# Performance work log

Measured on AMD Instinct MI355X. Metric: run time of the kernel, lower is better.

The kernel has to match this reference:

```python
import jax, jax.numpy as jnp
import numpy as np

B, T, D, H, V, L = 2, 1024, 512, 8, 50257, 4
HD = D // H  # head size
FF = 4 * D


def _ln(x, w, b):
    mu = jnp.mean(x, axis=-1, keepdims=True)
    var = jnp.mean((x - mu) ** 2, axis=-1, keepdims=True)
    return (x - mu) * jax.lax.rsqrt(var + 1e-5) * w + b


def setup_inputs() -> dict:
    key = jax.random.key(0)
    ks = jax.random.split(key, 12)
    s = 0.02
    return {
        "idx": jax.random.randint(ks[0], (B, T), 0, V),
        "tok_emb": jax.random.normal(ks[1], (V, D)) * s,
        "pos_emb": jax.random.normal(ks[2], (T, D)) * s,
        "Wq": jax.random.normal(ks[3], (L, H, D, HD)) * s,
        "Wk": jax.random.normal(ks[4], (L, H, D, HD)) * s,
        "Wv": jax.random.normal(ks[5], (L, H, D, HD)) * s,
        "Wo": jax.random.normal(ks[6], (L, D, D)) * s,
        "bo": jnp.zeros((L, D)),
        "W1": jax.random.normal(ks[7], (L, D, FF)) * s,
        "b1": jnp.zeros((L, FF)),
        "W2": jax.random.normal(ks[8], (L, FF, D)) * s,
        "b2": jnp.zeros((L, D)),
        "ln1_w": jnp.ones((L, D)), "ln1_b": jnp.zeros((L, D)),
        "ln2_w": jnp.ones((L, D)), "ln2_b": jnp.zeros((L, D)),
        "Wlm": jax.random.normal(ks[9], (D, V)) * s,
        "blm": jnp.zeros((V,)),
    }


def reference(idx, tok_emb, pos_emb, Wq, Wk, Wv, Wo, bo, W1, b1, W2, b2,
              ln1_w, ln1_b, ln2_w, ln2_b, Wlm, blm):
    b, t = idx.shape
    x = tok_emb[idx] + pos_emb[:t]  # [B,T,D]
    mask = jnp.tril(jnp.ones((t, t), dtype=bool))
    scale = D ** (-0.5)  # NOTE: original scales by full n_embd, not head_size
    for l in range(L):
        # pre-norm that also feeds the residual (x = ln1(x); x = x + sa(x))
        h = _ln(x, ln1_w[l], ln1_b[l])
        q = jnp.einsum('btd,hdk->bhtk', h, Wq[l])
        k = jnp.einsum('btd,hdk->bhtk', h, Wk[l])
        v = jnp.einsum('btd,hdk->bhtk', h, Wv[l])
        wei = jnp.einsum('bhtk,bhsk->bhts', q, k) * scale
        wei = jnp.where(mask, wei, -jnp.inf)
        wei = jax.nn.softmax(wei, axis=-1)  # dropout omitted (eval mode)
        att = jnp.einsum('bhts,bhsk->bhtk', wei, v)
        att = att.transpose(0, 2, 1, 3).reshape(b, t, D)  # concat heads
        x = h + att @ Wo[l] + bo[l]
        h2 = _ln(x, ln2_w[l], ln2_b[l])
        x = h2 + jax.nn.relu(h2 @ W1[l] + b1[l]) @ W2[l] + b2[l]
    logits = x @ Wlm + blm  # [B,T,V]
    return logits
```

## Files before the change

### kernel.cpp

```cpp
#include <hip/hip_runtime.h>
#include <hip/hip_bf16.h>

typedef __hip_bfloat16 bf16;
typedef __attribute__((ext_vector_type(8))) short s8v;
typedef __attribute__((ext_vector_type(4))) float f4v;

#define B_ 2
#define T_ 1024
#define D_ 512
#define H_ 8
#define HD_ 64
#define V_ 50257
#define VPAD_ 51200
#define L_ 4
#define FF_ 2048
#define BT_ (B_*T_)

__device__ __forceinline__ float ldw(const void* p, size_t i, int f32m) {
  return f32m ? ((const float*)p)[i] : __bfloat162float(((const bf16*)p)[i]);
}

__device__ __forceinline__ void gload_lds16(const void* g, void* l) {
  __builtin_amdgcn_global_load_lds((const __attribute__((address_space(1))) void*)g,
                                   (__attribute__((address_space(3))) void*)l, 16, 0, 0);
}

__global__ void detect_kernel(const void* __restrict__ ln1w, int* __restrict__ flag) {
  unsigned u = *(const unsigned*)ln1w;
  *flag = (u == 0x3F800000u) ? 1 : 0;
}

__global__ void embed_kernel(const int* __restrict__ idx, const void* __restrict__ tok,
                             const void* __restrict__ pos, float* __restrict__ x,
                             const int* __restrict__ flag) {
  int f32m = *flag;
  int i = blockIdx.x * 256 + threadIdx.x;
  int bt = i >> 9;
  int d  = i & (D_ - 1);
  int t  = bt & (T_ - 1);
  int tk = idx[bt];
  x[i] = ldw(tok, (size_t)tk * D_ + d, f32m) + ldw(pos, (size_t)t * D_ + d, f32m);
}

__global__ void ln_kernel(const float* __restrict__ x, const void* __restrict__ w,
                          const void* __restrict__ b, size_t eoff,
                          bf16* __restrict__ hb, float* __restrict__ hf,
                          const int* __restrict__ flag) {
  int f32m = *flag;
  int t = blockIdx.x;
  int tid = threadIdx.x;
  const float* row = x + (size_t)t * D_;
  float v0 = row[tid], v1 = row[tid + 256];
  __shared__ float red[256];
  red[tid] = v0 + v1;
  __syncthreads();
  for (int s = 128; s > 0; s >>= 1) { if (tid < s) red[tid] += red[tid + s]; __syncthreads(); }
  float mu = red[0] * (1.f / D_);
  __syncthreads();
  float d0 = v0 - mu, d1 = v1 - mu;
  red[tid] = d0 * d0 + d1 * d1;
  __syncthreads();
  for (int s = 128; s > 0; s >>= 1) { if (tid < s) red[tid] += red[tid + s]; __syncthreads(); }
  float rs = rsqrtf(red[0] * (1.f / D_) + 1e-5f);
  float o0 = d0 * rs * ldw(w, eoff + tid, f32m)       + ldw(b, eoff + tid, f32m);
  float o1 = d1 * rs * ldw(w, eoff + tid + 256, f32m) + ldw(b, eoff + tid + 256, f32m);
  size_t base = (size_t)t * D_;
  hf[base + tid] = o0;        hf[base + tid + 256] = o1;
  hb[base + tid] = __float2bfloat16(o0);
  hb[base + tid + 256] = __float2bfloat16(o1);
}

__global__ void repack_qkv_all_kernel(const void* __restrict__ Wq, const void* __restrict__ Wk,
                                      const void* __restrict__ Wv, bf16* __restrict__ out,
                                      const int* __restrict__ flag) {
  int f32m = *flag;
  int zz = blockIdx.z;
  size_t eoff = (size_t)zz * H_ * D_ * HD_;
  out += (size_t)zz * 1536 * 512;
  int i = blockIdx.x * 256 + threadIdx.x;
  int n = i >> 9, k = i & 511;
  int sel = n >> 9; int cc = n & 511; int hh = cc >> 6; int hd = cc & 63;
  const void* src = (sel == 0) ? Wq : (sel == 1) ? Wk : Wv;
  out[i] = __float2bfloat16(ldw(src, eoff + ((size_t)hh * D_ + k) * HD_ + hd, f32m));
}

__global__ void repack_qkv_kernel(const void* __restrict__ Wq, const void* __restrict__ Wk,
                                  const void* __restrict__ Wv, size_t eoff,
                                  bf16* __restrict__ out, const int* __restrict__ flag) {
  int f32m = *flag;
  int i = blockIdx.x * 256 + threadIdx.x;
  int n = i >> 9, k = i & 511;
  int sel = n >> 9; int cc = n & 511; int hh = cc >> 6; int hd = cc & 63;
  const void* src = (sel == 0) ? Wq : (sel == 1) ? Wk : Wv;
  out[i] = __float2bfloat16(ldw(src, eoff + ((size_t)hh * D_ + k) * HD_ + hd, f32m));
}

__global__ void transpose_kernel(const void* __restrict__ in, size_t eoff,
                                 bf16* __restrict__ out, int K, int Nin,
                                 const int* __restrict__ flag) {
  int f32m = *flag;
  __shared__ bf16 tl[32][33];
  int n0 = blockIdx.x * 32, k0 = blockIdx.y * 32;
  int tx = threadIdx.x & 31, ty = threadIdx.x >> 5;
#pragma unroll
  for (int i = 0; i < 4; ++i) {
    int k = k0 + ty + i * 8;
    int n = n0 + tx;
    float v = (n < Nin) ? ldw(in, eoff + (size_t)k * Nin + n, f32m) : 0.f;
    tl[ty + i * 8][tx] = __float2bfloat16(v);
  }
  __syncthreads();
#pragma unroll
  for (int i = 0; i < 4; ++i) {
    int n = n0 + ty + i * 8;
    out[(size_t)n * K + k0 + tx] = tl[tx][ty + i * 8];
  }
}

__global__ void transpose_all_kernel(const void* __restrict__ in,
                                     bf16* __restrict__ out,
                                     int K, int Nin, const int* __restrict__ flag) {
  int f32m = *flag;
  int zz = blockIdx.z;
  size_t eoff = (size_t)zz * K * Nin;
  out += (size_t)zz * Nin * K;
  __shared__ bf16 tl[32][33];
  int n0 = blockIdx.x * 32, k0 = blockIdx.y * 32;
  int tx = threadIdx.x & 31, ty = threadIdx.x >> 5;
#pragma unroll
  for (int i = 0; i < 4; ++i) {
    int k = k0 + ty + i * 8;
    int n = n0 + tx;
    tl[ty + i * 8][tx] = __float2bfloat16(ldw(in, eoff + (size_t)k * Nin + n, f32m));
  }
  __syncthreads();
#pragma unroll
  for (int i = 0; i < 4; ++i) {
    int n = n0 + ty + i * 8;
    out[(size_t)n * K + k0 + tx] = tl[tx][ty + i * 8];
  }
}

template<int OUTM, int BIAS, int RES, int RELU, int XB>
__global__ __launch_bounds__(256)
void mfma_gemm64(const bf16* __restrict__ A, const bf16* __restrict__ Bt,
                 void* __restrict__ Cout, const void* __restrict__ bias, size_t bieoff,
                 const float* __restrict__ res, bf16* __restrict__ xb2,
                 const int* __restrict__ flag, int M, int Nc, int K) {
  __shared__ __align__(16) short As[2][2048];
  __shared__ __align__(16) short Bs[2][2048];
  const int tid = threadIdx.x;
  const int brow = blockIdx.x * 64;
  const int bcol = blockIdx.y * 64;
  const int w = tid >> 6, lane = tid & 63;
  const int wr = w >> 1, wc = w & 1;
  const int lr = lane & 15, lk = lane >> 4;

  const int e0 = tid * 8;
  const int r0 = e0 >> 5;
  const int c0 = (e0 & 31) ^ ((r0 & 3) << 3);
  const bf16* ag0 = A + (size_t)(brow + r0) * K + c0;
  const bf16* bg0 = Bt + (size_t)(bcol + r0) * K + c0;

  int aoff[2], boff[2];
#pragma unroll
  for (int i = 0; i < 2; ++i) {
    int ra = wr * 32 + i * 16 + lr;
    aoff[i] = ra * 32 + ((lk * 8) ^ ((lr & 3) << 3));
    int rb = wc * 32 + i * 16 + lr;
    boff[i] = rb * 32 + ((lk * 8) ^ ((lr & 3) << 3));
  }

  f4v acc[2][2];
  const f4v z = {0.f, 0.f, 0.f, 0.f};
#pragma unroll
  for (int i = 0; i < 2; ++i)
#pragma unroll
    for (int j = 0; j < 2; ++j) acc[i][j] = z;

  const int nt = K >> 5;
  gload_lds16(ag0, &As[0][e0]);
  gload_lds16(bg0, &Bs[0][e0]);

  for (int kt = 0; kt < nt; ++kt) {
    __syncthreads();
    const int cur = kt & 1;
    if (kt + 1 < nt) {
      const size_t ko = (size_t)(kt + 1) * 32;
      gload_lds16(ag0 + ko, &As[cur ^ 1][e0]);
      gload_lds16(bg0 + ko, &Bs[cur ^ 1][e0]);
    }
    s8v a[2], b[2];
#pragma unroll
    for (int i = 0; i < 2; ++i) a[i] = *(const s8v*)&As[cur][aoff[i]];
#pragma unroll
    for (int i = 0; i < 2; ++i) b[i] = *(const s8v*)&Bs[cur][boff[i]];
#pragma unroll
    for (int mi = 0; mi < 2; ++mi)
#pragma unroll
      for (int ni = 0; ni < 2; ++ni)
        acc[mi][ni] = __builtin_amdgcn_mfma_f32_16x16x32_bf16(a[mi], b[ni], acc[mi][ni], 0, 0, 0);
  }

  const int f32m = *flag;
#pragma unroll
  for (int mi = 0; mi < 2; ++mi) {
    const int row = brow + wr * 32 + mi * 16 + lk * 4;
#pragma unroll
    for (int ni = 0; ni < 2; ++ni) {
      const int col = bcol + wc * 32 + ni * 16 + lr;
      if (col < Nc) {
        float bv = BIAS ? ldw(bias, bieoff + col, f32m) : 0.f;
#pragma unroll
        for (int rr = 0; rr < 4; ++rr) {
          float v = acc[mi][ni][rr] + bv;
          size_t ci = (size_t)(row + rr) * Nc + col;
          if (RES) v += res[ci];
          if (RELU) v = fmaxf(v, 0.f);
          if (OUTM == 0) ((float*)Cout)[ci] = v;
          else           ((bf16*)Cout)[ci] = __float2bfloat16(v);
          if (XB) xb2[ci] = __float2bfloat16(v);
        }
      }
    }
  }
}

__global__ __launch_bounds__(512, 1)
void mfma_gemm_lm256(const bf16* __restrict__ A, const bf16* __restrict__ Bt,
                     void* __restrict__ Cout, const void* __restrict__ bias,
                     const int* __restrict__ flag, int M, int Nc) {
  const int K = 512;
  __shared__ __align__(16) short As[4][8192];
  __shared__ __align__(16) short Bs[4][8192];
  const int bid = blockIdx.x;
  const int xcd = bid & 7;
  const int chunk = bid >> 3;
  const int brow = (chunk & 7) * 256;
  const int bcol = (xcd * 25 + (chunk >> 3)) * 256;
  const int tid = threadIdx.x;
  const int w = tid >> 6, lane = tid & 63;
  const int wr = w >> 2, wc = w & 3;
  const int lr = lane & 15, lk = lane >> 4;

  const int e0 = tid * 8, e1 = 4096 + tid * 8;
  const int r0 = e0 >> 5, r1 = e1 >> 5;
  const int c0 = (e0 & 31) ^ (((r0 >> 1) & 3) << 3);
  const int c1 = (e1 & 31) ^ (((r1 >> 1) & 3) << 3);
  const bf16* ag0 = A + (size_t)(brow + r0) * K + c0;
  const bf16* ag1 = A + (size_t)(brow + r1) * K + c1;
  const bf16* bg0 = Bt + (size_t)(bcol + r0) * K + c0;
  const bf16* bg1 = Bt + (size_t)(bcol + r1) * K + c1;

  int aoff[8], boff[4];
#pragma unroll
  for (int mi = 0; mi < 8; ++mi) {
    int ra = wr * 128 + mi * 16 + lr;
    aoff[mi] = ra * 32 + ((lk * 8) ^ (((ra >> 1) & 3) << 3));
  }
#pragma unroll
  for (int ni = 0; ni < 4; ++ni) {
    int rb = wc * 64 + ni * 16 + lr;
    boff[ni] = rb * 32 + ((lk * 8) ^ (((rb >> 1) & 3) << 3));
  }

  f4v acc[8][4];
  const f4v z = {0.f, 0.f, 0.f, 0.f};
#pragma unroll
  for (int i = 0; i < 8; ++i)
#pragma unroll
    for (int j = 0; j < 4; ++j) acc[i][j] = z;

#pragma unroll
  for (int t = 0; t < 3; ++t) {
    const size_t ko = (size_t)t * 32;
    gload_lds16(ag0 + ko, &As[t][e0]); gload_lds16(ag1 + ko, &As[t][e1]);
    gload_lds16(bg0 + ko, &Bs[t][e0]); gload_lds16(bg1 + ko, &Bs[t][e1]);
  }

  for (int kt = 0; kt < 16; ++kt) {
    if (kt < 14)       asm volatile("s_waitcnt vmcnt(8)" ::: "memory");
    else if (kt == 14) asm volatile("s_waitcnt vmcnt(4)" ::: "memory");
    else               asm volatile("s_waitcnt vmcnt(0)" ::: "memory");
    __builtin_amdgcn_s_barrier();
    __builtin_amdgcn_sched_barrier(0);
    const int cur = kt & 3;
    if (kt + 3 < 16) {
      const int nb = (kt + 3) & 3;
      const size_t ko = (size_t)(kt + 3) * 32;
      gload_lds16(ag0 + ko, &As[nb][e0]); gload_lds16(ag1 + ko, &As[nb][e1]);
      gload_lds16(bg0 + ko, &Bs[nb][e0]); gload_lds16(bg1 + ko, &Bs[nb][e1]);
    }
    s8v a[8], b[4];
#pragma unroll
    for (int i = 0; i < 8; ++i) a[i] = *(const s8v*)&As[cur][aoff[i]];
#pragma unroll
    for (int i = 0; i < 4; ++i) b[i] = *(const s8v*)&Bs[cur][boff[i]];
    __builtin_amdgcn_s_setprio(1);
#pragma unroll
    for (int mi = 0; mi < 8; ++mi)
#pragma unroll
      for (int ni = 0; ni < 4; ++ni)
        acc[mi][ni] = __builtin_amdgcn_mfma_f32_16x16x32_bf16(a[mi], b[ni], acc[mi][ni], 0, 0, 0);
    __builtin_amdgcn_s_setprio(0);
  }

  const int f32m = *flag;
#pragma unroll
  for (int mi = 0; mi < 8; ++mi) {
    const int row = brow + wr * 128 + mi * 16 + lk * 4;
#pragma unroll
    for (int ni = 0; ni < 4; ++ni) {
      const int col = bcol + wc * 64 + ni * 16 + lr;
      if (col < Nc) {
        float bv = ldw(bias, col, f32m);
#pragma unroll
        for (int rr = 0; rr < 4; ++rr) {
          float v = acc[mi][ni][rr] + bv;
          size_t ci = (size_t)(row + rr) * Nc + col;
          if (f32m) ((float*)Cout)[ci] = v;
          else      ((bf16*)Cout)[ci] = __float2bfloat16(v);
        }
      }
    }
  }
}

#define ATT_SCALE 0.044194173824159216f
__global__ __launch_bounds__(128) void fattn_kernel(const bf16* __restrict__ qkv,
                                                    bf16* __restrict__ att) {
  const int tid = threadIdx.x;
  const int w = tid >> 6, lane = tid & 63;
  const int lr = lane & 15, lk = lane >> 4;
  const int sx = blockIdx.x;
  const int strip = (sx & 1) ? (31 - (sx >> 1)) : (sx >> 1);
  const int s0 = strip * 32;
  const int hh = blockIdx.y, b = blockIdx.z;
  const int q0w = s0 + w * 16;

  __shared__ __align__(16) short Klds[64 * 64];
  __shared__ __align__(16) short Vt[64 * 72];
  __shared__ __align__(16) short Pl[2][16 * 72];
  unsigned* vt32 = (unsigned*)Vt;

  const bf16* qbase = qkv + (size_t)(b * T_ + q0w + lr) * 1536 + hh * 64;
  s8v qf[2];
#pragma unroll
  for (int kk = 0; kk < 2; ++kk)
    qf[kk] = *(const s8v*)(qbase + kk * 32 + lk * 8);

  const bf16* kg = qkv + (size_t)b * T_ * 1536 + 512 + hh * 64;
  const bf16* vg = kg + 512;

  f4v acc_o[4];
  const f4v z4 = {0.f, 0.f, 0.f, 0.f};
#pragma unroll
  for (int dt = 0; dt < 4; ++dt) acc_o[dt] = z4;
  float m[4], l[4];
#pragma unroll
  for (int r = 0; r < 4; ++r) { m[r] = -1e30f; l[r] = 0.f; }

  const int jmax = (s0 + 31) >> 6;
  for (int jt = 0; jt <= jmax; ++jt) {
    __syncthreads();
    const bf16* kt = kg + (size_t)jt * 64 * 1536;
#pragma unroll
    for (int c = 0; c < 4; ++c) {
      int e = tid * 8 + c * 1024;
      int row = e >> 6, col = e & 63;
      int colw = col ^ ((row & 7) << 3);
      gload_lds16(kt + (size_t)row * 1536 + colw, &Klds[e]);
    }
    const bf16* vgt = vg + (size_t)jt * 64 * 1536;
#pragma unroll
    for (int u = 0; u < 2; ++u) {
      int unit = tid * 2 + u;
      int kp = unit >> 3, cc = (unit & 7) * 8;
      s8v v0 = *(const s8v*)(vgt + (size_t)(2 * kp) * 1536 + cc);
      s8v v1 = *(const s8v*)(vgt + (size_t)(2 * kp + 1) * 1536 + cc);
#pragma unroll
      for (int j = 0; j < 8; ++j) {
        unsigned pk = (unsigned)(unsigned short)v0[j] |
                      ((unsigned)(unsigned short)v1[j] << 16);
        vt32[(cc + j) * 36 + kp] = pk;
      }
    }
    __syncthreads();

    if (jt * 64 <= q0w + 15) {
      const bool diag = (jt == jmax);
      f4v s[4];
#pragma unroll
      for (int nt = 0; nt < 4; ++nt) s[nt] = z4;
#pragma unroll
      for (int kk = 0; kk < 2; ++kk)
#pragma unroll
        for (int nt = 0; nt < 4; ++nt) {
          int row = nt * 16 + lr;
          const s8v kf = *(const s8v*)&Klds[row * 64 +
                           ((kk * 32 + lk * 8) ^ ((lr & 7) << 3))];
          s[nt] = __builtin_amdgcn_mfma_f32_16x16x32_bf16(qf[kk], kf, s[nt], 0, 0, 0);
        }
      float pv[4][4];
#pragma unroll
      for (int nt = 0; nt < 4; ++nt)
#pragma unroll
        for (int r = 0; r < 4; ++r) {
          float v = s[nt][r] * ATT_SCALE;
          if (diag && (jt * 64 + nt * 16 + lr > q0w + lk * 4 + r)) v = -1e30f;
          pv[nt][r] = v;
        }
#pragma unroll
      for (int r = 0; r < 4; ++r) {
        float mm = fmaxf(fmaxf(pv[0][r], pv[1][r]), fmaxf(pv[2][r], pv[3][r]));
        mm = fmaxf(mm, __shfl_xor(mm, 1));
        mm = fmaxf(mm, __shfl_xor(mm, 2));
        mm = fmaxf(mm, __shfl_xor(mm, 4));
        mm = fmaxf(mm, __shfl_xor(mm, 8));
        float nm = fmaxf(m[r], mm);
        float cf = __expf(m[r] - nm);
        m[r] = nm;
        float ls = 0.f;
#pragma unroll
        for (int nt = 0; nt < 4; ++nt) {
          float p = __expf(pv[nt][r] - nm);
          pv[nt][r] = p;
          ls += p;
        }
        ls += __shfl_xor(ls, 1); ls += __shfl_xor(ls, 2);
        ls += __shfl_xor(ls, 4); ls += __shfl_xor(ls, 8);
        l[r] = l[r] * cf + ls;
#pragma unroll
        for (int dt = 0; dt < 4; ++dt) acc_o[dt][r] *= cf;
      }
      bf16* pw = (bf16*)&Pl[w][0];
#pragma unroll
      for (int nt = 0; nt < 4; ++nt)
#pragma unroll
        for (int r = 0; r < 4; ++r)
          pw[(lk * 4 + r) * 72 + nt * 16 + lr] = __float2bfloat16(pv[nt][r]);
#pragma unroll
      for (int kk = 0; kk < 2; ++kk) {
        const s8v pa = *(const s8v*)&Pl[w][lr * 72 + kk * 32 + lk * 8];
#pragma unroll
        for (int dt = 0; dt < 4; ++dt) {
          const s8v vf = *(const s8v*)&Vt[(dt * 16 + lr) * 72 + kk * 32 + lk * 8];
          acc_o[dt] = __builtin_amdgcn_mfma_f32_16x16x32_bf16(pa, vf, acc_o[dt], 0, 0, 0);
        }
      }
    }
  }

#pragma unroll
  for (int dt = 0; dt < 4; ++dt)
#pragma unroll
    for (int r = 0; r < 4; ++r) {
      int q = q0w + lk * 4 + r;
      float v = acc_o[dt][r] / l[r];
      att[(size_t)(b * T_ + q) * D_ + hh * 64 + dt * 16 + lr] = __float2bfloat16(v);
    }
}

__global__ void cast_kernel(const float* __restrict__ x, bf16* __restrict__ xb) {
  int i = blockIdx.x * 256 + threadIdx.x;
  xb[i] = __float2bfloat16(x[i]);
}

__global__ void lm_fallback_kernel(const float* __restrict__ A, const void* __restrict__ Bw,
                                   void* __restrict__ Cout, const void* __restrict__ bias,
                                   const int* __restrict__ flag, int M, int N, int K) {
  const int f32m = *flag;
  __shared__ __align__(16) float As[16][72];
  __shared__ __align__(16) float Bs[16][72];
  const int tid = threadIdx.x;
  const int brow = blockIdx.y * 64;
  const int bcol = blockIdx.x * 64;
  const int tr = tid >> 4, tc = tid & 15;
  float acc[4][4] = {};
  for (int k0 = 0; k0 < K; k0 += 16) {
#pragma unroll
    for (int i = 0; i < 4; ++i) {
      int e = tid + i * 256;
      int r = e >> 4, c = e & 15;
      As[c][r] = A[(size_t)(brow + r) * K + k0 + c];
    }
#pragma unroll
    for (int i = 0; i < 4; ++i) {
      int e = tid + i * 256;
      int r = e >> 6, c = e & 63;
      int col = bcol + c;
      Bs[r][c] = (col < N) ? ldw(Bw, (size_t)(k0 + r) * N + col, f32m) : 0.f;
    }
    __syncthreads();
#pragma unroll
    for (int kk = 0; kk < 16; ++kk) {
      const float4 av = *reinterpret_cast<const float4*>(&As[kk][tr * 4]);
      const float4 bv = *reinterpret_cast<const float4*>(&Bs[kk][tc * 4]);
      float a_[4] = {av.x, av.y, av.z, av.w};
      float b_[4] = {bv.x, bv.y, bv.z, bv.w};
#pragma unroll
      for (int i = 0; i < 4; ++i)
#pragma unroll
        for (int j = 0; j < 4; ++j) acc[i][j] += a_[i] * b_[j];
    }
    __syncthreads();
  }
#pragma unroll
  for (int i = 0; i < 4; ++i) {
    int row = brow + tr * 4 + i;
#pragma unroll
    for (int j = 0; j < 4; ++j) {
      int col = bcol + tc * 4 + j;
      if (col < N) {
        float v = acc[i][j] + ldw(bias, col, f32m);
        if (f32m) ((float*)Cout)[(size_t)row * N + col] = v;
        else      ((bf16*) Cout)[(size_t)row * N + col] = __float2bfloat16(v);
      }
    }
  }
}

template<int OUTM, int BI, int RE, int RL, int XB>
static void launch_g64(const bf16* A, const bf16* Bt, void* C, const void* bias,
                       size_t bieoff, const float* res, bf16* xb2, const int* flag,
                       int M, int Nc, int Npad, int K, hipStream_t s) {
  dim3 grid(M / 64, Npad / 64);
  mfma_gemm64<OUTM, BI, RE, RL, XB><<<grid, 256, 0, s>>>(A, Bt, C, bias, bieoff, res,
                                                         xb2, flag, M, Nc, K);
}

extern "C" void kernel_launch(void* const* d_in, const int* in_sizes, int n_in,
                              void* d_out, int out_size, void* d_ws, size_t ws_size,
                              hipStream_t stream) {
  const int*  idx  = (const int*) d_in[0];
  const void* tok  = d_in[1];
  const void* pos  = d_in[2];
  const void* Wq   = d_in[3];
  const void* Wk   = d_in[4];
  const void* Wv   = d_in[5];
  const void* Wo   = d_in[6];
  const void* bo   = d_in[7];
  const void* W1   = d_in[8];
  const void* b1   = d_in[9];
  const void* W2   = d_in[10];
  const void* b2   = d_in[11];
  const void* ln1w = d_in[12];
  const void* ln1b = d_in[13];
  const void* ln2w = d_in[14];
  const void* ln2b = d_in[15];
  const void* Wlm  = d_in[16];
  const void* blm  = d_in[17];

  char* p = (char*)d_ws;
  int*   flag = (int*)p;            p += 256;
  float* x    = (float*)p;          p += (size_t)BT_ * D_ * 4;
  float* hf   = (float*)p;          p += (size_t)BT_ * D_ * 4;
  bf16*  h    = (bf16*)p;           p += (size_t)BT_ * D_ * 2;
  bf16*  R    = (bf16*)p;           p += (size_t)BT_ * FF_ * 2;
  bf16*  qkvP = (bf16*)p;           p += (size_t)L_ * 1536 * 512 * 2;
  bf16*  woP  = (bf16*)p;           p += (size_t)L_ * 512 * 512 * 2;
  bf16*  w1P  = (bf16*)p;           p += (size_t)L_ * 2048 * 512 * 2;
  bf16*  w2P  = (bf16*)p;           p += (size_t)L_ * 512 * 2048 * 2;
  bf16*  wlmP = (bf16*)p;
  size_t need_all = (size_t)(p - (char*)d_ws) + (size_t)VPAD_ * D_ * 2;
  bf16*  wrep = qkvP;
  bf16*  wlmF = (bf16*)((char*)qkvP + (size_t)FF_ * D_ * 2);
  size_t need_old = ((char*)wlmF - (char*)d_ws) + (size_t)VPAD_ * D_ * 2;

  bf16* qkv = R;
  bf16* att = R + (size_t)BT_ * 1536;
  bf16* ff  = R;
  bf16* xb  = h;

  detect_kernel<<<1, 1, 0, stream>>>(ln1w, flag);
  embed_kernel<<<BT_ * D_ / 256, 256, 0, stream>>>(idx, tok, pos, x, flag);

  if (ws_size >= need_all) {
    repack_qkv_all_kernel<<<dim3(1536 * 512 / 256, 1, L_), 256, 0, stream>>>(
        Wq, Wk, Wv, qkvP, flag);
    transpose_all_kernel<<<dim3(16, 16, L_), 256, 0, stream>>>(Wo, woP, 512, 512, flag);
    transpose_all_kernel<<<dim3(64, 16, L_), 256, 0, stream>>>(W1, w1P, 512, 2048, flag);
    transpose_all_kernel<<<dim3(16, 64, L_), 256, 0, stream>>>(W2, w2P, 2048, 512, flag);
    transpose_kernel<<<dim3(VPAD_ / 32, 16), 256, 0, stream>>>(Wlm, 0, wlmP, 512, V_, flag);

    for (int l = 0; l < L_; ++l) {
      ln_kernel<<<BT_, 256, 0, stream>>>(x, ln1w, ln1b, (size_t)l * D_, h, hf, flag);
      launch_g64<1,0,0,0,0>(h, qkvP + (size_t)l * 1536 * 512, qkv, nullptr, 0, nullptr,
                            nullptr, flag, BT_, 1536, 1536, 512, stream);
      fattn_kernel<<<dim3(32, H_, B_), 128, 0, stream>>>(qkv, att);
      launch_g64<0,1,1,0,0>(att, woP + (size_t)l * 512 * 512, x, bo, (size_t)l * D_, hf,
                            nullptr, flag, BT_, 512, 512, 512, stream);
      ln_kernel<<<BT_, 256, 0, stream>>>(x, ln2w, ln2b, (size_t)l * D_, h, hf, flag);
      launch_g64<1,1,0,1,0>(h, w1P + (size_t)l * 2048 * 512, ff, b1, (size_t)l * FF_,
                            nullptr, nullptr, flag, BT_, 2048, 2048, 512, stream);
      if (l < L_ - 1)
        launch_g64<0,1,1,0,0>(ff, w2P + (size_t)l * 512 * 2048, x, b2, (size_t)l * D_, hf,
                              nullptr, flag, BT_, 512, 512, 2048, stream);
      else
        launch_g64<0,1,1,0,1>(ff, w2P + (size_t)l * 512 * 2048, x, b2, (size_t)l * D_, hf,
                              xb, flag, BT_, 512, 512, 2048, stream);
    }
    mfma_gemm_lm256<<<(BT_ / 256) * (VPAD_ / 256), 512, 0, stream>>>(
        xb, wlmP, d_out, blm, flag, BT_, V_);
  } else {
    const bool big = ws_size >= need_old;
    for (int l = 0; l < L_; ++l) {
      ln_kernel<<<BT_, 256, 0, stream>>>(x, ln1w, ln1b, (size_t)l * D_, h, hf, flag);
      repack_qkv_kernel<<<1536 * 512 / 256, 256, 0, stream>>>(
          Wq, Wk, Wv, (size_t)l * H_ * D_ * HD_, wrep, flag);
      launch_g64<1,0,0,0,0>(h, wrep, qkv, nullptr, 0, nullptr, nullptr, flag,
                            BT_, 1536, 1536, 512, stream);
      fattn_kernel<<<dim3(32, H_, B_), 128, 0, stream>>>(qkv, att);
      transpose_kernel<<<dim3(16, 16), 256, 0, stream>>>(Wo, (size_t)l * D_ * D_, wrep, 512, 512, flag);
      launch_g64<0,1,1,0,0>(att, wrep, x, bo, (size_t)l * D_, hf, nullptr, flag,
                            BT_, 512, 512, 512, stream);
      ln_kernel<<<BT_, 256, 0, stream>>>(x, ln2w, ln2b, (size_t)l * D_, h, hf, flag);
      transpose_kernel<<<dim3(64, 16), 256, 0, stream>>>(W1, (size_t)l * D_ * FF_, wrep, 512, 2048, flag);
      launch_g64<1,1,0,1,0>(h, wrep, ff, b1, (size_t)l * FF_, nullptr, nullptr, flag,
                            BT_, 2048, 2048, 512, stream);
      transpose_kernel<<<dim3(16, 64), 256, 0, stream>>>(W2, (size_t)l * FF_ * D_, wrep, 2048, 512, flag);
      launch_g64<0,1,1,0,0>(ff, wrep, x, b2, (size_t)l * D_, hf, nullptr, flag,
                            BT_, 512, 512, 2048, stream);
    }
    if (big) {
      cast_kernel<<<BT_ * D_ / 256, 256, 0, stream>>>(x, xb);
      transpose_kernel<<<dim3(VPAD_ / 32, 16), 256, 0, stream>>>(Wlm, 0, wlmF, 512, V_, flag);
      mfma_gemm_lm256<<<(BT_ / 256) * (VPAD_ / 256), 512, 0, stream>>>(
          xb, wlmF, d_out, blm, flag, BT_, V_);
    } else {
      lm_fallback_kernel<<<dim3((V_ + 63) / 64, BT_ / 64), 256, 0, stream>>>(
          x, Wlm, d_out, blm, flag, BT_, V_, 512);
    }
  }
}
```

Baseline: 776.1 us.

## Split LM-head GEMM k-step into four phases interleaving LDS reads, prefetch, MFMA

Restructures the LM-head GEMM inner loop so each k-step runs as four phases. Each phase reads two A fragments from LDS, issues one of the four global-to-LDS prefetch loads, then runs 8 MFMAs, with barriers between phases. The goal is to overlap LDS reads and global prefetches with matrix math and to cut register pressure from holding all 8 A fragments at once. In exchange it adds many s_barriers per k-step, which could stall the waves.

After: 768.0 us. Within noise of the previous version (-1.0%).

```diff
diff --git a/kernel.cpp b/kernel.cpp
--- a/kernel.cpp
+++ b/kernel.cpp
@@ -278,32 +278,74 @@
     gload_lds16(bg0 + ko, &Bs[t][e0]); gload_lds16(bg1 + ko, &Bs[t][e1]);
   }
 
+#define LM_MFMA_PAIR(P, A0, A1)                                                     \
+    acc[2*(P)][0]   = __builtin_amdgcn_mfma_f32_16x16x32_bf16(A0, b0, acc[2*(P)][0], 0, 0, 0);   \
+    acc[2*(P)][1]   = __builtin_amdgcn_mfma_f32_16x16x32_bf16(A0, b1, acc[2*(P)][1], 0, 0, 0);   \
+    acc[2*(P)][2]   = __builtin_amdgcn_mfma_f32_16x16x32_bf16(A0, b2, acc[2*(P)][2], 0, 0, 0);   \
+    acc[2*(P)][3]   = __builtin_amdgcn_mfma_f32_16x16x32_bf16(A0, b3, acc[2*(P)][3], 0, 0, 0);   \
+    acc[2*(P)+1][0] = __builtin_amdgcn_mfma_f32_16x16x32_bf16(A1, b0, acc[2*(P)+1][0], 0, 0, 0); \
+    acc[2*(P)+1][1] = __builtin_amdgcn_mfma_f32_16x16x32_bf16(A1, b1, acc[2*(P)+1][1], 0, 0, 0); \
+    acc[2*(P)+1][2] = __builtin_amdgcn_mfma_f32_16x16x32_bf16(A1, b2, acc[2*(P)+1][2], 0, 0, 0); \
+    acc[2*(P)+1][3] = __builtin_amdgcn_mfma_f32_16x16x32_bf16(A1, b3, acc[2*(P)+1][3], 0, 0, 0)
+
   for (int kt = 0; kt < 16; ++kt) {
+    const int cur = kt & 3;
+    const int nb = (kt + 3) & 3;
+    const size_t ko = (size_t)(kt + 3) * 32;
+    const bool pf = (kt + 3 < 16);
+
     if (kt < 14)       asm volatile("s_waitcnt vmcnt(8)" ::: "memory");
     else if (kt == 14) asm volatile("s_waitcnt vmcnt(4)" ::: "memory");
     else               asm volatile("s_waitcnt vmcnt(0)" ::: "memory");
     __builtin_amdgcn_s_barrier();
+    s8v b0 = *(const s8v*)&Bs[cur][boff[0]];
+    s8v b1 = *(const s8v*)&Bs[cur][boff[1]];
+    s8v b2 = *(const s8v*)&Bs[cur][boff[2]];
+    s8v b3 = *(const s8v*)&Bs[cur][boff[3]];
+    s8v a0 = *(const s8v*)&As[cur][aoff[0]];
+    s8v a1 = *(const s8v*)&As[cur][aoff[1]];
+    if (pf) gload_lds16(ag0 + ko, &As[nb][e0]);
+    asm volatile("s_waitcnt lgkmcnt(0)" ::: "memory");
     __builtin_amdgcn_sched_barrier(0);
-    const int cur = kt & 3;
-    if (kt + 3 < 16) {
-      const int nb = (kt + 3) & 3;
-      const size_t ko = (size_t)(kt + 3) * 32;
-      gload_lds16(ag0 + ko, &As[nb][e0]); gload_lds16(ag1 + ko, &As[nb][e1]);
-      gload_lds16(bg0 + ko, &Bs[nb][e0]); gload_lds16(bg1 + ko, &Bs[nb][e1]);
-    }
-    s8v a[8], b[4];
-#pragma unroll
-    for (int i = 0; i < 8; ++i) a[i] = *(const s8v*)&As[cur][aoff[i]];
-#pragma unroll
-    for (int i = 0; i < 4; ++i) b[i] = *(const s8v*)&Bs[cur][boff[i]];
     __builtin_amdgcn_s_setprio(1);
-#pragma unroll
-    for (int mi = 0; mi < 8; ++mi)
-#pragma unroll
-      for (int ni = 0; ni < 4; ++ni)
-        acc[mi][ni] = __builtin_amdgcn_mfma_f32_16x16x32_bf16(a[mi], b[ni], acc[mi][ni], 0, 0, 0);
+    LM_MFMA_PAIR(0, a0, a1);
     __builtin_amdgcn_s_setprio(0);
-  }
+    __builtin_amdgcn_s_barrier();
+
+    a0 = *(const s8v*)&As[cur][aoff[2]];
+    a1 = *(const s8v*)&As[cur][aoff[3]];
+    if (pf) gload_lds16(ag1 + ko, &As[nb][e1]);
+    __builtin_amdgcn_s_barrier();
+    asm volatile("s_waitcnt lgkmcnt(0)" ::: "memory");
+    __builtin_amdgcn_sched_barrier(0);
+    __builtin_amdgcn_s_setprio(1);
+    LM_MFMA_PAIR(1, a0, a1);
+    __builtin_amdgcn_s_setprio(0);
+    __builtin_amdgcn_s_barrier();
+
+    a0 = *(const s8v*)&As[cur][aoff[4]];
+    a1 = *(const s8v*)&As[cur][aoff[5]];
+    if (pf) gload_lds16(bg0 + ko, &Bs[nb][e0]);
+    __builtin_amdgcn_s_barrier();
+    asm volatile("s_waitcnt lgkmcnt(0)" ::: "memory");
+    __builtin_amdgcn_sched_barrier(0);
+    __builtin_amdgcn_s_setprio(1);
+    LM_MFMA_PAIR(2, a0, a1);
+    __builtin_amdgcn_s_setprio(0);
+    __builtin_amdgcn_s_barrier();
+
+    a0 = *(const s8v*)&As[cur][aoff[6]];
+    a1 = *(const s8v*)&As[cur][aoff[7]];
+    if (pf) gload_lds16(bg1 + ko, &Bs[nb][e1]);
+    __builtin_amdgcn_s_barrier();
+    asm volatile("s_waitcnt lgkmcnt(0)" ::: "memory");
+    __builtin_amdgcn_sched_barrier(0);
+    __builtin_amdgcn_s_setprio(1);
+    LM_MFMA_PAIR(3, a0, a1);
+    __builtin_amdgcn_s_setprio(0);
+    __builtin_amdgcn_s_barrier();
+  }
+#undef LM_MFMA_PAIR
 
   const int f32m = *flag;
 #pragma unroll
```

## Retile LM-head GEMM to 256x128 blocks with 64-wide K steps and split prefetch

Applied to the files above, without the earlier changes.

The LM-head GEMM kernel changes from 256x256 output tiles with 32-wide K slices and a 4-stage buffer to 256x128 tiles with 64-wide K slices and a 3-stage buffer. Waves now form a 4x2 grid, each holding 4x4 accumulators instead of 8x4, and each K step is split into two halves with the prefetch loads interleaved between them. The XOR swizzle is redone for 64-element rows. This doubles the number of blocks, which should give more parallelism and lower register pressure, at the cost of more A-tile reloads and extra barriers per iteration.

New measurement: 787.5 us. No clear change (+1.5%).

```diff
diff --git a/kernel.cpp b/kernel.cpp
--- a/kernel.cpp
+++ b/kernel.cpp
@@ -231,84 +231,158 @@
                      void* __restrict__ Cout, const void* __restrict__ bias,
                      const int* __restrict__ flag, int M, int Nc) {
   const int K = 512;
-  __shared__ __align__(16) short As[4][8192];
-  __shared__ __align__(16) short Bs[4][8192];
+  __shared__ __align__(16) short As[3][16384];
+  __shared__ __align__(16) short Bs[3][8192];
   const int bid = blockIdx.x;
   const int xcd = bid & 7;
   const int chunk = bid >> 3;
   const int brow = (chunk & 7) * 256;
-  const int bcol = (xcd * 25 + (chunk >> 3)) * 256;
+  const int bcol = (xcd * 50 + (chunk >> 3)) * 128;
   const int tid = threadIdx.x;
   const int w = tid >> 6, lane = tid & 63;
-  const int wr = w >> 2, wc = w & 3;
+  const int wr = w >> 1, wc = w & 1;
   const int lr = lane & 15, lk = lane >> 4;
 
-  const int e0 = tid * 8, e1 = 4096 + tid * 8;
-  const int r0 = e0 >> 5, r1 = e1 >> 5;
-  const int c0 = (e0 & 31) ^ (((r0 >> 1) & 3) << 3);
-  const int c1 = (e1 & 31) ^ (((r1 >> 1) & 3) << 3);
-  const bf16* ag0 = A + (size_t)(brow + r0) * K + c0;
-  const bf16* ag1 = A + (size_t)(brow + r1) * K + c1;
-  const bf16* bg0 = Bt + (size_t)(bcol + r0) * K + c0;
-  const bf16* bg1 = Bt + (size_t)(bcol + r1) * K + c1;
-
-  int aoff[8], boff[4];
-#pragma unroll
-  for (int mi = 0; mi < 8; ++mi) {
-    int ra = wr * 128 + mi * 16 + lr;
-    aoff[mi] = ra * 32 + ((lk * 8) ^ (((ra >> 1) & 3) << 3));
+  int arow[4], acsw[4], brow_[2], bcsw[2];
+#pragma unroll
+  for (int c = 0; c < 4; ++c) {
+    int e = tid * 8 + c * 4096;
+    arow[c] = e >> 6;
+    acsw[c] = (e & 63) ^ ((arow[c] & 7) << 3);
+  }
+#pragma unroll
+  for (int c = 0; c < 2; ++c) {
+    int e = tid * 8 + c * 4096;
+    brow_[c] = e >> 6;
+    bcsw[c] = (e & 63) ^ ((brow_[c] & 7) << 3);
+  }
+  const bf16* agp[4]; const bf16* bgp[2];
+#pragma unroll
+  for (int c = 0; c < 4; ++c) agp[c] = A + (size_t)(brow + arow[c]) * K + acsw[c];
+#pragma unroll
+  for (int c = 0; c < 2; ++c) bgp[c] = Bt + (size_t)(bcol + brow_[c]) * K + bcsw[c];
+
+  int aoff[4][2], boff[4][2];
+#pragma unroll
+  for (int mi = 0; mi < 4; ++mi) {
+    int ra = wr * 64 + mi * 16 + lr;
+#pragma unroll
+    for (int kk = 0; kk < 2; ++kk)
+      aoff[mi][kk] = ra * 64 + ((kk * 32 + lk * 8) ^ ((lr & 7) << 3));
   }
 #pragma unroll
   for (int ni = 0; ni < 4; ++ni) {
     int rb = wc * 64 + ni * 16 + lr;
-    boff[ni] = rb * 32 + ((lk * 8) ^ (((rb >> 1) & 3) << 3));
-  }
-
-  f4v acc[8][4];
+#pragma unroll
+    for (int kk = 0; kk < 2; ++kk)
+      boff[ni][kk] = rb * 64 + ((kk * 32 + lk * 8) ^ ((lr & 7) << 3));
+  }
+
+  f4v acc[4][4];
   const f4v z = {0.f, 0.f, 0.f, 0.f};
 #pragma unroll
-  for (int i = 0; i < 8; ++i)
+  for (int i = 0; i < 4; ++i)
 #pragma unroll
     for (int j = 0; j < 4; ++j) acc[i][j] = z;
 
 #pragma unroll
-  for (int t = 0; t < 3; ++t) {
-    const size_t ko = (size_t)t * 32;
-    gload_lds16(ag0 + ko, &As[t][e0]); gload_lds16(ag1 + ko, &As[t][e1]);
-    gload_lds16(bg0 + ko, &Bs[t][e0]); gload_lds16(bg1 + ko, &Bs[t][e1]);
-  }
-
-  for (int kt = 0; kt < 16; ++kt) {
-    if (kt < 14)       asm volatile("s_waitcnt vmcnt(8)" ::: "memory");
-    else if (kt == 14) asm volatile("s_waitcnt vmcnt(4)" ::: "memory");
-    else               asm volatile("s_waitcnt vmcnt(0)" ::: "memory");
+  for (int t = 0; t < 2; ++t) {
+    const size_t ko = (size_t)t * 64;
+    const int e = tid * 8;
+#pragma unroll
+    for (int c = 0; c < 4; ++c) gload_lds16(agp[c] + ko, &As[t][e + c * 4096]);
+#pragma unroll
+    for (int c = 0; c < 2; ++c) gload_lds16(bgp[c] + ko, &Bs[t][e + c * 4096]);
+  }
+
+  int cur = 0;
+  for (int kt = 0; kt < 8; ++kt) {
+    const bool pf = (kt + 2 < 8);
+    int nb = cur + 2; if (nb >= 3) nb -= 3;
+    const size_t ko = (size_t)(kt + 2) * 64;
+    const int e = tid * 8;
+
+    if (kt < 7) asm volatile("s_waitcnt vmcnt(6)" ::: "memory");
+    else        asm volatile("s_waitcnt vmcnt(0)" ::: "memory");
     __builtin_amdgcn_s_barrier();
+    s8v a0 = *(const s8v*)&As[cur][aoff[0][0]];
+    s8v a1 = *(const s8v*)&As[cur][aoff[1][0]];
+    s8v a2 = *(const s8v*)&As[cur][aoff[2][0]];
+    s8v a3 = *(const s8v*)&As[cur][aoff[3][0]];
+    s8v b0 = *(const s8v*)&Bs[cur][boff[0][0]];
+    s8v b1 = *(const s8v*)&Bs[cur][boff[1][0]];
+    s8v b2 = *(const s8v*)&Bs[cur][boff[2][0]];
+    s8v b3 = *(const s8v*)&Bs[cur][boff[3][0]];
+    if (pf) {
+      gload_lds16(agp[0] + ko, &As[nb][e]);
+      gload_lds16(agp[1] + ko, &As[nb][e + 4096]);
+      gload_lds16(agp[2] + ko, &As[nb][e + 8192]);
+    }
+    asm volatile("s_waitcnt lgkmcnt(0)" ::: "memory");
     __builtin_amdgcn_sched_barrier(0);
-    const int cur = kt & 3;
-    if (kt + 3 < 16) {
-      const int nb = (kt + 3) & 3;
-      const size_t ko = (size_t)(kt + 3) * 32;
-      gload_lds16(ag0 + ko, &As[nb][e0]); gload_lds16(ag1 + ko, &As[nb][e1]);
-      gload_lds16(bg0 + ko, &Bs[nb][e0]); gload_lds16(bg1 + ko, &Bs[nb][e1]);
-    }
-    s8v a[8], b[4];
-#pragma unroll
-    for (int i = 0; i < 8; ++i) a[i] = *(const s8v*)&As[cur][aoff[i]];
-#pragma unroll
-    for (int i = 0; i < 4; ++i) b[i] = *(const s8v*)&Bs[cur][boff[i]];
     __builtin_amdgcn_s_setprio(1);
-#pragma unroll
-    for (int mi = 0; mi < 8; ++mi)
-#pragma unroll
-      for (int ni = 0; ni < 4; ++ni)
-        acc[mi][ni] = __builtin_amdgcn_mfma_f32_16x16x32_bf16(a[mi], b[ni], acc[mi][ni], 0, 0, 0);
+    acc[0][0] = __builtin_amdgcn_mfma_f32_16x16x32_bf16(a0, b0, acc[0][0], 0, 0, 0);
+    acc[0][1] = __builtin_amdgcn_mfma_f32_16x16x32_bf16(a0, b1, acc[0][1], 0, 0, 0);
+    acc[0][2] = __builtin_amdgcn_mfma_f32_16x16x32_bf16(a0, b2, acc[0][2], 0, 0, 0);
+    acc[0][3] = __builtin_amdgcn_mfma_f32_16x16x32_bf16(a0, b3, acc[0][3], 0, 0, 0);
+    acc[1][0] = __builtin_amdgcn_mfma_f32_16x16x32_bf16(a1, b0, acc[1][0], 0, 0, 0);
+    acc[1][1] = __builtin_amdgcn_mfma_f32_16x16x32_bf16(a1, b1, acc[1][1], 0, 0, 0);
+    acc[1][2] = __builtin_amdgcn_mfma_f32_16x16x32_bf16(a1, b2, acc[1][2], 0, 0, 0);
+    acc[1][3] = __builtin_amdgcn_mfma_f32_16x16x32_bf16(a1, b3, acc[1][3], 0, 0, 0);
+    acc[2][0] = __builtin_amdgcn_mfma_f32_16x16x32_bf16(a2, b0, acc[2][0], 0, 0, 0);
+    acc[2][1] = __builtin_amdgcn_mfma_f32_16x16x32_bf16(a2, b1, acc[2][1], 0, 0, 0);
+    acc[2][2] = __builtin_amdgcn_mfma_f32_16x16x32_bf16(a2, b2, acc[2][2], 0, 0, 0);
+    acc[2][3] = __builtin_amdgcn_mfma_f32_16x16x32_bf16(a2, b3, acc[2][3], 0, 0, 0);
+    acc[3][0] = __builtin_amdgcn_mfma_f32_16x16x32_bf16(a3, b0, acc[3][0], 0, 0, 0);
+    acc[3][1] = __builtin_amdgcn_mfma_f32_16x16x32_bf16(a3, b1, acc[3][1], 0, 0, 0);
+    acc[3][2] = __builtin_amdgcn_mfma_f32_16x16x32_bf16(a3, b2, acc[3][2], 0, 0, 0);
+    acc[3][3] = __builtin_amdgcn_mfma_f32_16x16x32_bf16(a3, b3, acc[3][3], 0, 0, 0);
     __builtin_amdgcn_s_setprio(0);
+    __builtin_amdgcn_s_barrier();
+
+    a0 = *(const s8v*)&As[cur][aoff[0][1]];
+    a1 = *(const s8v*)&As[cur][aoff[1][1]];
+    a2 = *(const s8v*)&As[cur][aoff[2][1]];
+    a3 = *(const s8v*)&As[cur][aoff[3][1]];
+    b0 = *(const s8v*)&Bs[cur][boff[0][1]];
+    b1 = *(const s8v*)&Bs[cur][boff[1][1]];
+    b2 = *(const s8v*)&Bs[cur][boff[2][1]];
+    b3 = *(const s8v*)&Bs[cur][boff[3][1]];
+    if (pf) {
+      gload_lds16(agp[3] + ko, &As[nb][e + 12288]);
+      gload_lds16(bgp[0] + ko, &Bs[nb][e]);
+      gload_lds16(bgp[1] + ko, &Bs[nb][e + 4096]);
+    }
+    __builtin_amdgcn_s_barrier();
+    asm volatile("s_waitcnt lgkmcnt(0)" ::: "memory");
+    __builtin_amdgcn_sched_barrier(0);
+    __builtin_amdgcn_s_setprio(1);
+    acc[0][0] = __builtin_amdgcn_mfma_f32_16x16x32_bf16(a0, b0, acc[0][0], 0, 0, 0);
+    acc[0][1] = __builtin_amdgcn_mfma_f32_16x16x32_bf16(a0, b1, acc[0][1], 0, 0, 0);
+    acc[0][2] = __builtin_amdgcn_mfma_f32_16x16x32_bf16(a0, b2, acc[0][2], 0, 0, 0);
+    acc[0][3] = __builtin_amdgcn_mfma_f32_16x16x32_bf16(a0, b3, acc[0][3], 0, 0, 0);
+    acc[1][0] = __builtin_amdgcn_mfma_f32_16x16x32_bf16(a1, b0, acc[1][0], 0, 0, 0);
+    acc[1][1] = __builtin_amdgcn_mfma_f32_16x16x32_bf16(a1, b1, acc[1][1], 0, 0, 0);
+    acc[1][2] = __builtin_amdgcn_mfma_f32_16x16x32_bf16(a1, b2, acc[1][2], 0, 0, 0);
+    acc[1][3] = __builtin_amdgcn_mfma_f32_16x16x32_bf16(a1, b3, acc[1][3], 0, 0, 0);
+    acc[2][0] = __builtin_amdgcn_mfma_f32_16x16x32_bf16(a2, b0, acc[2][0], 0, 0, 0);
+    acc[2][1] = __builtin_amdgcn_mfma_f32_16x16x32_bf16(a2, b1, acc[2][1], 0, 0, 0);
+    acc[2][2] = __builtin_amdgcn_mfma_f32_16x16x32_bf16(a2, b2, acc[2][2], 0, 0, 0);
+    acc[2][3] = __builtin_amdgcn_mfma_f32_16x16x32_bf16(a2, b3, acc[2][3], 0, 0, 0);
+    acc[3][0] = __builtin_amdgcn_mfma_f32_16x16x32_bf16(a3, b0, acc[3][0], 0, 0, 0);
+    acc[3][1] = __builtin_amdgcn_mfma_f32_16x16x32_bf16(a3, b1, acc[3][1], 0, 0, 0);
+    acc[3][2] = __builtin_amdgcn_mfma_f32_16x16x32_bf16(a3, b2, acc[3][2], 0, 0, 0);
+    acc[3][3] = __builtin_amdgcn_mfma_f32_16x16x32_bf16(a3, b3, acc[3][3], 0, 0, 0);
+    __builtin_amdgcn_s_setprio(0);
+    __builtin_amdgcn_s_barrier();
+
+    cur = (cur == 2) ? 0 : cur + 1;
   }
 
   const int f32m = *flag;
 #pragma unroll
-  for (int mi = 0; mi < 8; ++mi) {
-    const int row = brow + wr * 128 + mi * 16 + lk * 4;
+  for (int mi = 0; mi < 4; ++mi) {
+    const int row = brow + wr * 64 + mi * 16 + lk * 4;
 #pragma unroll
     for (int ni = 0; ni < 4; ++ni) {
       const int col = bcol + wc * 64 + ni * 16 + lr;
@@ -600,7 +674,7 @@
         launch_g64<0,1,1,0,1>(ff, w2P + (size_t)l * 512 * 2048, x, b2, (size_t)l * D_, hf,
                               xb, flag, BT_, 512, 512, 2048, stream);
     }
-    mfma_gemm_lm256<<<(BT_ / 256) * (VPAD_ / 256), 512, 0, stream>>>(
+    mfma_gemm_lm256<<<8 * (VPAD_ / 128), 512, 0, stream>>>(
         xb, wlmP, d_out, blm, flag, BT_, V_);
   } else {
     const bool big = ws_size >= need_old;
@@ -625,8 +699,8 @@
     if (big) {
       cast_kernel<<<BT_ * D_ / 256, 256, 0, stream>>>(x, xb);
       transpose_kernel<<<dim3(VPAD_ / 32, 16), 256, 0, stream>>>(Wlm, 0, wlmF, 512, V_, flag);
-      mfma_gemm_lm256<<<(BT_ / 256) * (VPAD_ / 256), 512, 0, stream>>>(
-          xb, wlmF, d_out, blm, flag, BT_, V_);
+      mfma_gemm_lm256<<<8 * (VPAD_ / 128), 512, 0, stream>>>(
+          x != nullptr ? xb : xb, wlmF, d_out, blm, flag, BT_, V_);
     } else {
       lm_fallback_kernel<<<dim3((V_ + 63) / 64, BT_ / 64), 256, 0, stream>>>(
           x, Wlm, d_out, blm, flag, BT_, V_, 512);
```
